# Kernel tuning notes

Hardware: AMD Instinct MI355X
Metric: run time of the kernel (lower is better)

## Reference

```python
import jax, jax.numpy as jnp
import numpy as np

B, T, D = 2, 2048, 1024
HV, HK = 16, 8
DK, DV = 64, 64
K_DIM = HK * DK          # 512
V_DIM = HV * DV          # 1024
CONV_DIM = 2 * K_DIM + V_DIM  # 2048
KS = 4                   # short-conv kernel size
EPS = 1e-6               # rms_norm_eps / l2norm eps


def setup_inputs() -> dict:
    key = jax.random.key(0)
    ks = jax.random.split(key, 9)
    g = lambda k, shape, sc: (jax.random.normal(k, shape, jnp.float32) * sc)
    return {
        "hidden_states": g(ks[0], (B, T, D), 1.0),
        "W_qkv": g(ks[1], (D, CONV_DIM), 0.02),
        "W_z": g(ks[2], (D, V_DIM), 0.02),
        "W_b": g(ks[3], (D, HV), 0.02),
        "W_a": g(ks[4], (D, HV), 0.02),
        "dt_bias": jnp.ones((HV,), jnp.float32),
        "A_log": jnp.log(jax.random.uniform(ks[5], (HV,), jnp.float32, 1e-3, 16.0)),
        "conv_w": g(ks[6], (CONV_DIM, KS), 0.2),
        "norm_w": jnp.ones((DV,), jnp.float32),
        "W_out": g(ks[7], (V_DIM, D), 0.02),
    }


def _causal_conv_silu(x, w):
    # depthwise causal conv1d over time, followed by SiLU (FLA ShortConvolution default)
    # x: [B,T,C], w: [C,KS]
    xp = jnp.pad(x, ((0, 0), (KS - 1, 0), (0, 0)))
    y = sum(xp[:, i:i + x.shape[1], :] * w[:, i] for i in range(KS))
    return jax.nn.silu(y)


def _l2norm(x):
    return x * jax.lax.rsqrt(jnp.sum(x * x, -1, keepdims=True) + EPS)


def _forward(hidden_states, W_qkv, W_z, W_b, W_a, dt_bias, A_log, conv_w, norm_w, W_out):
    b_, t_ = hidden_states.shape[:2]
    mixed_qkv = hidden_states @ W_qkv                       # [B,T,conv_dim]
    z = (hidden_states @ W_z).reshape(b_, t_, HV, DV)       # gate branch
    beta = jax.nn.sigmoid(hidden_states @ W_b)              # [B,T,HV]
    g = -jnp.exp(A_log) * jax.nn.softplus(hidden_states @ W_a + dt_bias)  # [B,T,HV]

    mixed_qkv = _causal_conv_silu(mixed_qkv, conv_w)
    q, k, v = jnp.split(mixed_qkv, [K_DIM, 2 * K_DIM], axis=-1)
    q = q.reshape(b_, t_, HK, DK)
    k = k.reshape(b_, t_, HK, DK)
    v = v.reshape(b_, t_, HV, DV)
    # GQA expansion of q/k to the value-head count
    rep = HV // HK
    q = jnp.repeat(q, rep, axis=2)
    k = jnp.repeat(k, rep, axis=2)
    # l2-norm on q/k in kernel; q additionally scaled by 1/sqrt(dk)
    q = _l2norm(q) * (DK ** -0.5)
    k = _l2norm(k)

    # gated delta-rule recurrence over time (state S: [B,HV,DK,DV])
    qT = q.transpose(1, 0, 2, 3)
    kT = k.transpose(1, 0, 2, 3)
    vT = v.transpose(1, 0, 2, 3)
    gT = g.transpose(1, 0, 2)
    bT = beta.transpose(1, 0, 2)

    def step(S, xs):
        q_t, k_t, v_t, g_t, b_t = xs
        S = S * jnp.exp(g_t)[..., None, None]
        kv = jnp.einsum('bhk,bhkv->bhv', k_t, S)
        S = S + jnp.einsum('bhk,bhv->bhkv', k_t, (v_t - kv) * b_t[..., None])
        o_t = jnp.einsum('bhk,bhkv->bhv', q_t, S)
        return S, o_t

    S0 = jnp.zeros((b_, HV, DK, DV), jnp.float32)
    _, oT = jax.lax.scan(step, S0, (qT, kT, vT, gT, bT))
    o = oT.transpose(1, 0, 2, 3)                            # [B,T,HV,DV]

    # gated RMSNorm: rmsnorm(o) * weight * silu(z)
    var = jnp.mean(o * o, axis=-1, keepdims=True)
    o = o * jax.lax.rsqrt(var + EPS) * norm_w * jax.nn.silu(z)

    return o.reshape(b_, t_, V_DIM) @ W_out


def reference(hidden_states, W_qkv, W_z, W_b, W_a, dt_bias, A_log, conv_w, norm_w, W_out):
    return _forward(hidden_states, W_qkv, W_z, W_b, W_a, dt_bias, A_log, conv_w, norm_w, W_out)
```

## Files before the change

kernel.cpp:

```cpp
#include <hip/hip_runtime.h>
#include <hip/hip_bf16.h>


typedef unsigned short u16;
typedef float f32x4 __attribute__((ext_vector_type(4)));
typedef short bf16x8 __attribute__((ext_vector_type(8)));
typedef u16 u16x4 __attribute__((ext_vector_type(4)));
typedef const __attribute__((address_space(1))) void* gptr_t;
typedef __attribute__((address_space(3))) void* lptr_t;

#define B_    2
#define T_    2048
#define HV_   16
#define HK_   8
#define NC_   32
#define BT_   4096
#define QKVZ_ 3072
#define NCOL_ 3200

__device__ __forceinline__ u16 f2bf(float f) {
  return __builtin_bit_cast(u16, __float2bfloat16(f));
}
__device__ __forceinline__ float bf2f(u16 u) {
  return __bfloat162float(__builtin_bit_cast(__hip_bfloat16, u));
}
__device__ __forceinline__ float sigm(float x) { return 1.f / (1.f + __expf(-x)); }

__global__ __launch_bounds__(256) void k_cast_hs(const float* __restrict__ in,
                                                 u16* __restrict__ out) {
  int i = (blockIdx.x * 256 + threadIdx.x) * 4;
  float4 v = *(const float4*)(in + i);
  u16x4 o; o.x = f2bf(v.x); o.y = f2bf(v.y); o.z = f2bf(v.z); o.w = f2bf(v.w);
  *(u16x4*)(out + i) = o;
}

__global__ __launch_bounds__(256) void k_tcast(const float* __restrict__ src,
                                               u16* __restrict__ dst, int R, int C) {
  __shared__ float tile[32][33];
  int c0 = blockIdx.x * 32, r0 = blockIdx.y * 32;
  int cx = threadIdx.x & 31, ry = threadIdx.x >> 5;
#pragma unroll
  for (int j = 0; j < 4; ++j)
    tile[ry * 4 + j][cx] = src[(long)(r0 + ry * 4 + j) * C + c0 + cx];
  __syncthreads();
#pragma unroll
  for (int j = 0; j < 4; ++j)
    dst[(long)(c0 + ry * 4 + j) * R + r0 + cx] = f2bf(tile[cx][ry * 4 + j]);
}

__global__ __launch_bounds__(256) void k_wcatT(const float* __restrict__ Wqkv,
                                               const float* __restrict__ Wz,
                                               const float* __restrict__ Wb,
                                               const float* __restrict__ Wa,
                                               u16* __restrict__ dst) {
  __shared__ float tile[32][33];
  int n0 = blockIdx.x * 32, k0 = blockIdx.y * 32;
  int cx = threadIdx.x & 31, ry = threadIdx.x >> 5;
#pragma unroll
  for (int j = 0; j < 4; ++j) {
    int kk = k0 + ry * 4 + j;
    int n = n0 + cx;
    float v;
    if (n < 2048)      v = Wqkv[(long)kk * 2048 + n];
    else if (n < 3072) v = Wz[(long)kk * 1024 + (n - 2048)];
    else if (n < 3088) v = Wb[kk * 16 + (n - 3072)];
    else if (n < 3104) v = Wa[kk * 16 + (n - 3088)];
    else               v = 0.f;
    tile[ry * 4 + j][cx] = v;
  }
  __syncthreads();
#pragma unroll
  for (int j = 0; j < 4; ++j)
    dst[(long)(n0 + ry * 4 + j) * 1024 + k0 + cx] = f2bf(tile[cx][ry * 4 + j]);
}

__global__ __launch_bounds__(256) void k_gemm(const u16* __restrict__ A,
                                              const u16* __restrict__ Bt,
                                              u16* __restrict__ C0,
                                              float* __restrict__ C1,
                                              int M, int N, int K, int mode) {
  __shared__ u16 As[128 * 64];
  __shared__ u16 Bs[128 * 64];
  int tid = threadIdx.x;
  int wid = tid >> 6, lane = tid & 63;
  int row0 = blockIdx.y * 128, col0 = blockIdx.x * 128;
  int wr = wid >> 1, wc = wid & 1;
  f32x4 acc[4][4];
#pragma unroll
  for (int m = 0; m < 4; ++m)
#pragma unroll
    for (int n = 0; n < 4; ++n) acc[m][n] = (f32x4){0.f, 0.f, 0.f, 0.f};

  int srow = lane >> 3;
  int skoff = (lane & 7) * 8;

  for (int k0 = 0; k0 < K; k0 += 64) {
#pragma unroll
    for (int it = 0; it < 4; ++it) {
      int seg = wid * 4 + it;
      int r = seg * 8 + srow;
      const u16* gA = A + (long)(row0 + r) * K + k0 + skoff;
      const u16* gB = Bt + (long)(col0 + r) * K + k0 + skoff;
      __builtin_amdgcn_global_load_lds((gptr_t)gA, (lptr_t)(As + seg * 512), 16, 0, 0);
      __builtin_amdgcn_global_load_lds((gptr_t)gB, (lptr_t)(Bs + seg * 512), 16, 0, 0);
    }
    asm volatile("s_waitcnt vmcnt(0)" ::: "memory");
    __syncthreads();
#pragma unroll
    for (int ks = 0; ks < 2; ++ks) {
      bf16x8 af[4], bfr[4];
      int kk = ks * 32 + (lane >> 4) * 8;
      int rA = wr * 64 + (lane & 15);
      int rB = wc * 64 + (lane & 15);
#pragma unroll
      for (int m = 0; m < 4; ++m) af[m] = *(const bf16x8*)(As + (rA + m * 16) * 64 + kk);
#pragma unroll
      for (int n = 0; n < 4; ++n) bfr[n] = *(const bf16x8*)(Bs + (rB + n * 16) * 64 + kk);
#pragma unroll
      for (int m = 0; m < 4; ++m)
#pragma unroll
        for (int n = 0; n < 4; ++n)
          acc[m][n] = __builtin_amdgcn_mfma_f32_16x16x32_bf16(af[m], bfr[n], acc[m][n], 0, 0, 0);
    }
    __syncthreads();
  }
#pragma unroll
  for (int m = 0; m < 4; ++m)
#pragma unroll
    for (int n = 0; n < 4; ++n)
#pragma unroll
      for (int r = 0; r < 4; ++r) {
        int row = row0 + wr * 64 + m * 16 + (lane >> 4) * 4 + r;
        int col = col0 + wc * 64 + n * 16 + (lane & 15);
        float v = acc[m][n][r];
        if (mode == 0) {
          if (col < QKVZ_) C0[(long)row * QKVZ_ + col] = f2bf(v);
          else             C1[(long)row * 128 + (col - QKVZ_)] = v;
        } else {
          C1[(long)row * N + col] = v;
        }
      }
}

__global__ __launch_bounds__(64) void k_conv(const u16* __restrict__ qkvz,
                                             const float* __restrict__ ba,
                                             const float* __restrict__ convw,
                                             const float* __restrict__ Alog,
                                             const float* __restrict__ dtb,
                                             u16* __restrict__ qn, u16* __restrict__ kn,
                                             u16* __restrict__ vb,
                                             float* __restrict__ beta, float* __restrict__ gb) {
  int bt = blockIdx.x;
  int t = bt & 2047;
  int l = threadIdx.x;
  long rb = (long)bt * QKVZ_;
#pragma unroll 1
  for (int j = 0; j < 32; ++j) {
    int c = j * 64 + l;
    float4 w = *(const float4*)(convw + c * 4);
    float a = 0.f;
#pragma unroll
    for (int d = 0; d < 4; ++d) {
      int tt = t - 3 + d;
      float x = (tt >= 0) ? bf2f(qkvz[rb + (long)(tt - t) * QKVZ_ + c]) : 0.f;
      a += x * ((const float*)&w)[d];
    }
    float y = a * sigm(a);
    if (j < 16) {
      float ss = y * y;
#pragma unroll
      for (int m = 1; m < 64; m <<= 1) ss += __shfl_xor(ss, m);
      float sc = rsqrtf(ss + 1e-6f);
      if (j < 8) qn[((long)bt * 8 + j) * 64 + l] = f2bf(y * sc * 0.125f);
      else       kn[((long)bt * 8 + (j - 8)) * 64 + l] = f2bf(y * sc);
    } else {
      vb[((long)bt * 16 + (j - 16)) * 64 + l] = f2bf(y);
    }
  }
  if (l < 16) {
    float xb = ba[(long)bt * 128 + l];
    beta[bt * 16 + l] = sigm(xb);
    float xa = ba[(long)bt * 128 + 16 + l] + dtb[l];
    float sp = (xa > 20.f) ? xa : log1pf(__expf(xa));
    gb[bt * 16 + l] = -__expf(Alog[l]) * sp;
  }
}

__global__ __launch_bounds__(256) void k_cpk2(const u16* __restrict__ qn,
                                              const u16* __restrict__ kn,
                                              const u16* __restrict__ vb,
                                              const float* __restrict__ beta,
                                              const float* __restrict__ gb,
                                              float* __restrict__ Gbuf,
                                              u16* __restrict__ TKTb,
                                              u16* __restrict__ WlTb, u16* __restrict__ MTb,
                                              u16* __restrict__ Pb, u16* __restrict__ Bb) {
  int c = blockIdx.x, hv = blockIdx.y, b = blockIdx.z;
  int hk = hv >> 1;
  int bh = b * HV_ + hv;
  int tid = threadIdx.x;
  int wv = tid >> 6, lane = tid & 63;
  int frow = lane & 15, fk = (lane >> 4) * 8;

  __shared__ __align__(16) char smem[78848];
  u16* Ks   = (u16*)smem;
  u16* Qs   = (u16*)(smem + 9216);
  u16* Ktt  = Qs;
  u16* As_  = (u16*)(smem + 18432);
  u16* RHSt = (u16*)(smem + 27648);
  u16* Xt   = (u16*)(smem + 46080);
  u16* T4   = (u16*)(smem + 64512);
  u16* Yl   = (u16*)(smem + 68608);
  __shared__ float Gl[64];
  __shared__ float Bl[64];

  long tbase = (long)b * T_ + c * 64;
  long tile = ((long)bh * NC_ + c) * 4096;

  if (tid < 64) {
    Gl[tid] = gb[(tbase + tid) * HV_ + hv];
    Bl[tid] = beta[(tbase + tid) * HV_ + hv];
  }
  if (tid == 0) {
    float s = 0.f;
    for (int i = 0; i < 64; ++i) { s += Gl[i]; Gl[i] = s; }
  }
  if (tid < 64) Gbuf[((long)bh * NC_ + c) * 64 + tid] = Gl[tid];
  for (int e = tid; e < 4608; e += 256) ((float*)Xt)[e] = 0.f;
  for (int e = tid; e < 2560; e += 256) ((float*)Yl)[e] = 0.f;
  for (int e = tid; e < 4096; e += 256) {
    int i = e >> 6, k = e & 63;
    Ks[i * 72 + k] = kn[(tbase + i) * 512 + hk * 64 + k];
    Qs[i * 72 + k] = qn[(tbase + i) * 512 + hk * 64 + k];
  }
  __syncthreads();

  {
    bf16x8 aKs[2];
#pragma unroll
    for (int ks = 0; ks < 2; ++ks)
      aKs[ks] = *(const bf16x8*)&Ks[(wv * 16 + frow) * 72 + ks * 32 + fk];
    f32x4 accM[4], accA[4];
#pragma unroll
    for (int nt = 0; nt < 4; ++nt) { accM[nt] = (f32x4){0,0,0,0}; accA[nt] = (f32x4){0,0,0,0}; }
#pragma unroll
    for (int ks = 0; ks < 2; ++ks) {
#pragma unroll
      for (int nt = 0; nt < 4; ++nt) {
        bf16x8 bq = *(const bf16x8*)&Qs[(nt * 16 + frow) * 72 + ks * 32 + fk];
        bf16x8 bk = *(const bf16x8*)&Ks[(nt * 16 + frow) * 72 + ks * 32 + fk];
        accM[nt] = __builtin_amdgcn_mfma_f32_16x16x32_bf16(aKs[ks], bq, accM[nt], 0, 0, 0);
        accA[nt] = __builtin_amdgcn_mfma_f32_16x16x32_bf16(aKs[ks], bk, accA[nt], 0, 0, 0);
      }
    }
#pragma unroll
    for (int nt = 0; nt < 4; ++nt) {
      int i = nt * 16 + frow;
#pragma unroll
      for (int r = 0; r < 4; ++r) {
        int s = wv * 16 + (lane >> 4) * 4 + r;
        float val = (s <= i) ? accM[nt][r] * __expf(Gl[i] - Gl[s]) : 0.f;
        MTb[tile + s * 64 + i] = f2bf(val);
      }
    }
#pragma unroll
    for (int nt = 0; nt < 4; ++nt) {
      int s = nt * 16 + frow;
#pragma unroll
      for (int r = 0; r < 4; ++r) {
        int i = wv * 16 + (lane >> 4) * 4 + r;
        float val = (s < i) ? Bl[i] * __expf(Gl[i] - Gl[s]) * accA[nt][r] : 0.f;
        As_[i * 72 + s] = f2bf(val);
      }
    }
  }

  for (int e = tid; e < 4096; e += 256) {
    int i = e >> 6, v = e & 63;
    RHSt[v * 72 + i] = f2bf(Bl[i] * bf2f(vb[(tbase + i) * 1024 + hv * 64 + v]));
  }
  for (int e = tid; e < 4096; e += 256) {
    int i = e >> 6, k = e & 63;
    RHSt[(64 + k) * 72 + i] = f2bf(Bl[i] * __expf(Gl[i]) * bf2f(Ks[i * 72 + k]));
  }
  __syncthreads();

  {
    if (lane < 16) {
      int cc = lane;
      float Tc[16];
#pragma unroll
      for (int j = 0; j < 16; ++j) Tc[j] = (j == cc) ? 1.f : 0.f;
#pragma unroll
      for (int s = 0; s < 15; ++s)
#pragma unroll
        for (int i = s + 1; i < 16; ++i) {
          float a = bf2f(As_[(wv * 16 + i) * 72 + wv * 16 + s]);
          Tc[i] -= a * Tc[s];
        }
#pragma unroll
      for (int i = 0; i < 16; ++i) T4[(wv * 16 + i) * 32 + cc] = f2bf(Tc[i]);
    } else if (lane < 32) {
      int c2 = lane - 16;
#pragma unroll
      for (int i = 0; i < 16; ++i) T4[(wv * 16 + i) * 32 + 16 + c2] = 0;
    }
  }
  __syncthreads();

#pragma unroll 1
  for (int bb = 0; bb < 4; ++bb) {
    f32x4 uacc[2];
    uacc[0] = (f32x4){0,0,0,0}; uacc[1] = (f32x4){0,0,0,0};
#pragma unroll
    for (int ks = 0; ks < 2; ++ks) {
      bf16x8 bfr = *(const bf16x8*)&As_[(bb * 16 + frow) * 72 + ks * 32 + fk];
#pragma unroll
      for (int mt = 0; mt < 2; ++mt) {
        bf16x8 aa = *(const bf16x8*)&Xt[((wv * 2 + mt) * 16 + frow) * 72 + ks * 32 + fk];
        uacc[mt] = __builtin_amdgcn_mfma_f32_16x16x32_bf16(aa, bfr, uacc[mt], 0, 0, 0);
      }
    }
#pragma unroll
    for (int mt = 0; mt < 2; ++mt)
#pragma unroll
      for (int r = 0; r < 4; ++r) {
        int vr = (wv * 2 + mt) * 16 + (lane >> 4) * 4 + r;
        float y = bf2f(RHSt[vr * 72 + bb * 16 + frow]) - uacc[mt][r];
        Yl[vr * 40 + frow] = f2bf(y);
      }
    __syncthreads();
    {
      bf16x8 tb = *(const bf16x8*)&T4[(bb * 16 + frow) * 32 + fk];
      f32x4 zacc[2];
      zacc[0] = (f32x4){0,0,0,0}; zacc[1] = (f32x4){0,0,0,0};
#pragma unroll
      for (int mt = 0; mt < 2; ++mt) {
        bf16x8 aa = *(const bf16x8*)&Yl[((wv * 2 + mt) * 16 + frow) * 40 + fk];
        zacc[mt] = __builtin_amdgcn_mfma_f32_16x16x32_bf16(aa, tb, zacc[mt], 0, 0, 0);
      }
#pragma unroll
      for (int mt = 0; mt < 2; ++mt)
#pragma unroll
        for (int r = 0; r < 4; ++r) {
          int vr = (wv * 2 + mt) * 16 + (lane >> 4) * 4 + r;
          Xt[vr * 72 + bb * 16 + frow] = f2bf(zacc[mt][r]);
        }
    }
    __syncthreads();
  }

  float gend = Gl[63];
  for (int e = tid; e < 4096; e += 256) {
    int i = e >> 6, r = e & 63;
    Ktt[r * 72 + i] = f2bf(__expf(gend - Gl[i]) * bf2f(Ks[i * 72 + r]));
  }
#pragma unroll
  for (int t8 = 0; t8 < 2; ++t8) {
    int seg = tid + t8 * 256;
    int row = seg >> 2, s4 = (seg & 3) * 16;
    bf16x8 x0 = *(const bf16x8*)&Xt[row * 72 + s4];
    bf16x8 x1 = *(const bf16x8*)&Xt[row * 72 + s4 + 8];
    u16* dst = (row < 64) ? (WlTb + tile + row * 64 + s4)
                          : (TKTb + tile + (long)(row - 64) * 64 + s4);
    *(bf16x8*)dst = x0;
    *(bf16x8*)(dst + 8) = x1;
  }
  __syncthreads();

  {
    f32x4 acc[4];
#pragma unroll
    for (int nt = 0; nt < 4; ++nt) acc[nt] = (f32x4){0,0,0,0};
#pragma unroll
    for (int ks = 0; ks < 2; ++ks) {
      bf16x8 aa = *(const bf16x8*)&Ktt[(wv * 16 + frow) * 72 + ks * 32 + fk];
#pragma unroll
      for (int nt = 0; nt < 4; ++nt) {
        bf16x8 bfr = *(const bf16x8*)&Xt[(nt * 16 + frow) * 72 + ks * 32 + fk];
        acc[nt] = __builtin_amdgcn_mfma_f32_16x16x32_bf16(aa, bfr, acc[nt], 0, 0, 0);
      }
    }
#pragma unroll
    for (int nt = 0; nt < 4; ++nt) {
      int v = nt * 16 + frow;
#pragma unroll
      for (int r = 0; r < 4; ++r) {
        int rr = wv * 16 + (lane >> 4) * 4 + r;
        Bb[tile + rr * 64 + v] = f2bf(acc[nt][r]);
      }
    }
  }
  {
    f32x4 acc[4];
#pragma unroll
    for (int nt = 0; nt < 4; ++nt) acc[nt] = (f32x4){0,0,0,0};
#pragma unroll
    for (int ks = 0; ks < 2; ++ks) {
      bf16x8 aa = *(const bf16x8*)&Xt[(64 + wv * 16 + frow) * 72 + ks * 32 + fk];
#pragma unroll
      for (int nt = 0; nt < 4; ++nt) {
        bf16x8 bfr = *(const bf16x8*)&Ktt[(nt * 16 + frow) * 72 + ks * 32 + fk];
        acc[nt] = __builtin_amdgcn_mfma_f32_16x16x32_bf16(aa, bfr, acc[nt], 0, 0, 0);
      }
    }
#pragma unroll
    for (int nt = 0; nt < 4; ++nt) {
      int rr = nt * 16 + frow;
#pragma unroll
      for (int r = 0; r < 4; ++r) {
        int k2 = wv * 16 + (lane >> 4) * 4 + r;
        Pb[tile + k2 * 64 + rr] = f2bf(acc[nt][r]);
      }
    }
  }
}

__global__ __launch_bounds__(256) void k_seq2(const u16* __restrict__ Pb,
                                              const u16* __restrict__ Bb,
                                              const float* __restrict__ Gbuf,
                                              u16* __restrict__ Stb) {
  int vblk = blockIdx.x, bh = blockIdx.y;
  int tid = threadIdx.x;
  __shared__ u16 Abf[2][4096];
  __shared__ u16 Bbf[2][512];
  __shared__ float S_lds[64][10];
  __shared__ float gam[NC_];
  int i_ = tid & 63, vg = tid >> 6;
  int wv = tid >> 6, ln = tid & 63;
  if (tid < NC_) gam[tid] = __expf(Gbuf[((long)bh * NC_ + tid) * 64 + 63]);
  for (int e = tid; e < 640; e += 256) ((float*)S_lds)[e] = 0.f;
  float a0 = 0.f, a1 = 0.f;
  {
    long tl = (long)bh * NC_ * 4096;
    const u16* gA = Pb + tl + wv * 512 + ln * 8;
    __builtin_amdgcn_global_load_lds((gptr_t)gA, (lptr_t)&Abf[0][wv * 512], 16, 0, 0);
    __builtin_amdgcn_global_load_lds((gptr_t)(gA + 2048), (lptr_t)&Abf[0][2048 + wv * 512], 16, 0, 0);
    int ii = tid >> 2, vp = tid & 3;
    const u16* gB = Bb + tl + ii * 64 + vblk * 8 + vp * 2;
    __builtin_amdgcn_global_load_lds((gptr_t)gB, (lptr_t)&Bbf[0][wv * 128], 4, 0, 0);
  }
  for (int c = 0; c < NC_; ++c) {
    int cur = c & 1;
    asm volatile("s_waitcnt vmcnt(0)" ::: "memory");
    __syncthreads();
    if (c + 1 < NC_) {
      long tl = ((long)bh * NC_ + c + 1) * 4096;
      const u16* gA = Pb + tl + wv * 512 + ln * 8;
      __builtin_amdgcn_global_load_lds((gptr_t)gA, (lptr_t)&Abf[cur ^ 1][wv * 512], 16, 0, 0);
      __builtin_amdgcn_global_load_lds((gptr_t)(gA + 2048), (lptr_t)&Abf[cur ^ 1][2048 + wv * 512], 16, 0, 0);
      int ii = tid >> 2, vp = tid & 3;
      const u16* gB = Bb + tl + ii * 64 + vblk * 8 + vp * 2;
      __builtin_amdgcn_global_load_lds((gptr_t)gB, (lptr_t)&Bbf[cur ^ 1][wv * 128], 4, 0, 0);
    }
    {
      long stile = ((long)bh * NC_ + c) * 4096;
      int v0 = vblk * 8 + vg * 2;
      Stb[stile + (long)v0 * 64 + i_] = f2bf(a0);
      Stb[stile + (long)(v0 + 1) * 64 + i_] = f2bf(a1);
    }
    float g = gam[c];
    float n0 = 0.f, n1 = 0.f;
#pragma unroll 8
    for (int k = 0; k < 64; ++k) {
      float p = bf2f(Abf[cur][k * 64 + i_]);
      float2 sv = *(const float2*)&S_lds[k][vg * 2];
      n0 += p * sv.x;
      n1 += p * sv.y;
    }
    float b0 = bf2f(Bbf[cur][i_ * 8 + vg * 2]);
    float b1 = bf2f(Bbf[cur][i_ * 8 + vg * 2 + 1]);
    a0 = g * a0 - n0 + b0;
    a1 = g * a1 - n1 + b1;
    __syncthreads();
    S_lds[i_][vg * 2] = a0;
    S_lds[i_][vg * 2 + 1] = a1;
  }
}

__global__ __launch_bounds__(256) void k_ok2(const u16* __restrict__ MTb,
                                             const u16* __restrict__ TKTb,
                                             const u16* __restrict__ WlTb,
                                             const u16* __restrict__ Stb,
                                             const u16* __restrict__ qn,
                                             const float* __restrict__ Gbuf,
                                             float* __restrict__ O) {
  int c = blockIdx.x, hv = blockIdx.y, b = blockIdx.z;
  int bh = b * HV_ + hv, hk = hv >> 1;
  int tid = threadIdx.x;
  __shared__ float TKt[64][68];
  __shared__ float Ss[64][68];
  __shared__ float Ws[64][68];
  __shared__ float Qt[64][68];
  __shared__ float Gl[64];
  long tile = ((long)bh * NC_ + c) * 4096;
  long tbase = (long)b * T_ + c * 64;
  if (tid < 64) Gl[tid] = Gbuf[((long)bh * NC_ + c) * 64 + tid];
  __syncthreads();
  for (int e = tid; e < 4096; e += 256)
    TKt[e >> 6][e & 63] = bf2f(TKTb[tile + e]);
  for (int e = tid; e < 4096; e += 256) {
    int i = e >> 6, k = e & 63;
    Qt[k][i] = __expf(Gl[i]) * bf2f(qn[(tbase + i) * 512 + hk * 64 + k]);
  }
  for (int e = tid; e < 4096; e += 256) {
    int v = e >> 6, x = e & 63;
    Ss[x][v] = bf2f(Stb[tile + e]);
    Ws[x][v] = bf2f(WlTb[tile + e]);
  }
  __syncthreads();
  int tx = tid & 15, ty = tid >> 4;
  int i0 = ty * 4, v0 = tx * 4;
  float w[4][4];
#pragma unroll
  for (int r = 0; r < 4; ++r) *(f32x4*)w[r] = *(const f32x4*)&Ws[i0 + r][v0];
  for (int k = 0; k < 64; ++k) {
    f32x4 tk = *(const f32x4*)&TKt[k][i0];
    f32x4 sv = *(const f32x4*)&Ss[k][v0];
#pragma unroll
    for (int r = 0; r < 4; ++r)
#pragma unroll
      for (int q = 0; q < 4; ++q) w[r][q] -= tk[r] * sv[q];
  }
  __syncthreads();
#pragma unroll
  for (int r = 0; r < 4; ++r) *(f32x4*)&Ws[i0 + r][v0] = *(const f32x4*)w[r];
  for (int e = tid; e < 4096; e += 256)
    TKt[e >> 6][e & 63] = bf2f(MTb[tile + e]);
  __syncthreads();
  float o[4][4] = {};
  for (int s = 0; s < 64; ++s) {
    f32x4 mv = *(const f32x4*)&TKt[s][i0];
    f32x4 wv = *(const f32x4*)&Ws[s][v0];
#pragma unroll
    for (int r = 0; r < 4; ++r)
#pragma unroll
      for (int q = 0; q < 4; ++q) o[r][q] += mv[r] * wv[q];
  }
  for (int k = 0; k < 64; ++k) {
    f32x4 qv = *(const f32x4*)&Qt[k][i0];
    f32x4 sv = *(const f32x4*)&Ss[k][v0];
#pragma unroll
    for (int r = 0; r < 4; ++r)
#pragma unroll
      for (int q = 0; q < 4; ++q) o[r][q] += qv[r] * sv[q];
  }
#pragma unroll
  for (int r = 0; r < 4; ++r) {
    float4 o4 = make_float4(o[r][0], o[r][1], o[r][2], o[r][3]);
    *(float4*)&O[((tbase + i0 + r) * HV_ + hv) * 64 + v0] = o4;
  }
}

__global__ __launch_bounds__(256) void k_rms(const float* __restrict__ O,
                                             const u16* __restrict__ qkvz,
                                             const float* __restrict__ normw,
                                             u16* __restrict__ on) {
  int bt = blockIdx.x;
  int tid = threadIdx.x;
  __shared__ float ps[256];
  __shared__ float rstd[16];
  float4 o4 = *(const float4*)&O[(long)bt * 1024 + tid * 4];
  ps[tid] = o4.x * o4.x + o4.y * o4.y + o4.z * o4.z + o4.w * o4.w;
  __syncthreads();
  if (tid < 16) {
    float s = 0.f;
#pragma unroll
    for (int u = 0; u < 16; ++u) s += ps[tid * 16 + u];
    rstd[tid] = rsqrtf(s * (1.f / 64.f) + 1e-6f);
  }
  __syncthreads();
  float rs = rstd[tid >> 4];
  u16x4 ov;
#pragma unroll
  for (int j = 0; j < 4; ++j) {
    int idx = tid * 4 + j;
    float z = bf2f(qkvz[(long)bt * QKVZ_ + 2048 + idx]);
    float val = ((const float*)&o4)[j] * rs * normw[idx & 63] * (z * sigm(z));
    ((u16*)&ov)[j] = f2bf(val);
  }
  *(u16x4*)(on + (long)bt * 1024 + tid * 4) = ov;
}

extern "C" void kernel_launch(void* const* d_in, const int* in_sizes, int n_in,
                              void* d_out, int out_size, void* d_ws, size_t ws_size,
                              hipStream_t stream) {
  const float* hs    = (const float*)d_in[0];
  const float* Wqkv  = (const float*)d_in[1];
  const float* Wz    = (const float*)d_in[2];
  const float* Wb    = (const float*)d_in[3];
  const float* Wa    = (const float*)d_in[4];
  const float* dtb   = (const float*)d_in[5];
  const float* Alog  = (const float*)d_in[6];
  const float* convw = (const float*)d_in[7];
  const float* normw = (const float*)d_in[8];
  const float* Wout  = (const float*)d_in[9];
  float* out = (float*)d_out;

  char* p = (char*)d_ws;
  auto take = [&](size_t bytes) {
    char* q = p;
    p += (bytes + 255) & ~(size_t)255;
    return (void*)q;
  };
  u16*   qkvz  = (u16*)take((size_t)BT_ * QKVZ_ * 2);
  float* ba    = (float*)take((size_t)BT_ * 128 * 4);
  u16*   hsb   = (u16*)take((size_t)BT_ * 1024 * 2);
  u16*   wcatT = (u16*)take((size_t)NCOL_ * 1024 * 2);
  u16*   woutT = (u16*)take((size_t)1024 * 1024 * 2);
  u16*   qn    = (u16*)take((size_t)BT_ * 512 * 2);
  u16*   kn    = (u16*)take((size_t)BT_ * 512 * 2);
  u16*   vbuf  = (u16*)take((size_t)BT_ * 1024 * 2);
  float* beta  = (float*)take((size_t)BT_ * 16 * 4);
  float* gbuf  = (float*)take((size_t)BT_ * 16 * 4);
  float* Gcum  = (float*)take((size_t)1024 * 64 * 4);
  u16*   TKTb  = (u16*)take((size_t)1024 * 4096 * 2);
  u16*   WlTb  = (u16*)take((size_t)1024 * 4096 * 2);
  u16*   MTb   = (u16*)take((size_t)1024 * 4096 * 2);
  u16*   Pb    = (u16*)take((size_t)1024 * 4096 * 2);
  u16*   Bb    = (u16*)take((size_t)1024 * 4096 * 2);
  u16*   Stb   = (u16*)take((size_t)1024 * 4096 * 2);
  float* Obuf  = (float*)take((size_t)BT_ * 1024 * 4);
  u16*   onb   = (u16*)take((size_t)BT_ * 1024 * 2);

  k_cast_hs<<<dim3(4096), dim3(256), 0, stream>>>(hs, hsb);
  k_wcatT<<<dim3(100, 32), dim3(256), 0, stream>>>(Wqkv, Wz, Wb, Wa, wcatT);
  k_tcast<<<dim3(32, 32), dim3(256), 0, stream>>>(Wout, woutT, 1024, 1024);
  k_gemm<<<dim3(25, 32), dim3(256), 0, stream>>>(hsb, wcatT, qkvz, ba, 4096, NCOL_, 1024, 0);
  k_conv<<<dim3(4096), dim3(64), 0, stream>>>(qkvz, ba, convw, Alog, dtb, qn, kn, vbuf, beta, gbuf);
  k_cpk2<<<dim3(32, 16, 2), dim3(256), 0, stream>>>(qn, kn, vbuf, beta, gbuf, Gcum, TKTb, WlTb, MTb, Pb, Bb);
  k_seq2<<<dim3(8, 32), dim3(256), 0, stream>>>(Pb, Bb, Gcum, Stb);
  k_ok2<<<dim3(32, 16, 2), dim3(256), 0, stream>>>(MTb, TKTb, WlTb, Stb, qn, Gcum, Obuf);
  k_rms<<<dim3(4096), dim3(256), 0, stream>>>(Obuf, qkvz, normw, onb);
  k_gemm<<<dim3(8, 32), dim3(256), 0, stream>>>(onb, woutT, (u16*)nullptr, out, 4096, 1024, 1024, 1);
}
```

Before: 363.0 us.

## Replace input projection GEMM with 256x256 pipelined LDS-DMA MFMA kernel

```diff
diff --git a/kernel.cpp b/kernel.cpp
--- a/kernel.cpp
+++ b/kernel.cpp
@@ -16,7 +16,7 @@
 #define NC_   32
 #define BT_   4096
 #define QKVZ_ 3072
-#define NCOL_ 3200
+#define NPAD_ 3328
 
 __device__ __forceinline__ u16 f2bf(float f) {
   return __builtin_bit_cast(u16, __float2bfloat16(f));
@@ -74,11 +74,118 @@
     dst[(long)(n0 + ry * 4 + j) * 1024 + k0 + cx] = f2bf(tile[cx][ry * 4 + j]);
 }
 
+__global__ __launch_bounds__(512, 1) void k_g1(const u16* __restrict__ A,
+                                               const u16* __restrict__ Bt,
+                                               u16* __restrict__ C0,
+                                               float* __restrict__ C1) {
+  extern __shared__ u16 smem[];
+  const int K = 1024;
+  int tid = threadIdx.x;
+  int wv = tid >> 6, lane = tid & 63;
+  int wm = wv >> 2, wn = wv & 3;
+  int frow = lane & 15, kq = lane >> 4;
+  long row0 = blockIdx.y * 256, col0 = blockIdx.x * 256;
+
+  f32x4 acc[8][4];
+#pragma unroll
+  for (int m = 0; m < 8; ++m)
+#pragma unroll
+    for (int n = 0; n < 4; ++n) acc[m][n] = (f32x4){0.f, 0.f, 0.f, 0.f};
+
+  auto stage = [&](int ts, int js) {
+    if (ts >= 16) return;
+    int op = js & 1, ks = js >> 1;
+    u16* base = smem + op * 32768 + (ts & 1) * 16384 + ks * 8192;
+    const u16* gsrc = op ? Bt : A;
+    long grow0 = op ? col0 : row0;
+#pragma unroll
+    for (int l = 0; l < 2; ++l) {
+      int c = wv * 128 + l * 64 + lane;
+      int cp = c ^ (((c >> 5) & 1) << 1);
+      int r = cp >> 2, kc = (cp & 3) * 8;
+      const u16* g = gsrc + (grow0 + r) * K + ts * 64 + ks * 32 + kc;
+      __builtin_amdgcn_global_load_lds((gptr_t)g, (lptr_t)(base + (wv * 128 + l * 64) * 8), 16, 0, 0);
+    }
+  };
+
+#define VM8 asm volatile("s_waitcnt vmcnt(8)" ::: "memory")
+#define VM4 asm volatile("s_waitcnt vmcnt(4)" ::: "memory")
+#define VM0 asm volatile("s_waitcnt vmcnt(0)" ::: "memory")
+#define VMN
+
+#define PHASE(T, KS, MH, STS, SJS, VMW)                                           \
+  {                                                                               \
+    bf16x8 af[4], bfr[4];                                                         \
+    const u16* Ab = smem + ((T) & 1) * 16384 + (KS) * 8192;                       \
+    const u16* Bb = smem + 32768 + ((T) & 1) * 16384 + (KS) * 8192;               \
+    _Pragma("unroll") for (int mt = 0; mt < 4; ++mt) {                            \
+      int R = wm * 128 + (MH) * 64 + mt * 16 + frow;                              \
+      int lin = R * 64 + kq * 16;                                                 \
+      af[mt] = *(const bf16x8*)((const char*)Ab + (lin ^ (((R >> 3) & 1) << 5))); \
+    }                                                                             \
+    _Pragma("unroll") for (int nt = 0; nt < 4; ++nt) {                            \
+      int R = wn * 64 + nt * 16 + frow;                                           \
+      int lin = R * 64 + kq * 16;                                                 \
+      bfr[nt] = *(const bf16x8*)((const char*)Bb + (lin ^ (((R >> 3) & 1) << 5)));\
+    }                                                                             \
+    stage(STS, SJS);                                                              \
+    VMW;                                                                          \
+    __syncthreads();                                                              \
+    __builtin_amdgcn_s_setprio(1);                                                \
+    _Pragma("unroll") for (int mt = 0; mt < 4; ++mt)                              \
+      _Pragma("unroll") for (int nt = 0; nt < 4; ++nt)                            \
+        acc[(MH) * 4 + mt][nt] = __builtin_amdgcn_mfma_f32_16x16x32_bf16(         \
+            af[mt], bfr[nt], acc[(MH) * 4 + mt][nt], 0, 0, 0);                    \
+    __builtin_amdgcn_s_setprio(0);                                                \
+    __syncthreads();                                                              \
+  }
+
+  stage(0, 0); stage(0, 1); stage(0, 2); stage(0, 3);
+  stage(1, 0); stage(1, 1);
+  VM8;
+  __syncthreads();
+
+#pragma unroll 1
+  for (int t = 0; t < 14; ++t) {
+    PHASE(t, 0, 0, t + 1, 2, VMN);
+    PHASE(t, 0, 1, t + 1, 3, VM8);
+    PHASE(t, 1, 0, t + 2, 0, VMN);
+    PHASE(t, 1, 1, t + 2, 1, VM8);
+  }
+  {
+    int t = 14;
+    PHASE(t, 0, 0, 15, 2, VMN);
+    PHASE(t, 0, 1, 15, 3, VM8);
+    PHASE(t, 1, 0, 16, 0, VMN);
+    PHASE(t, 1, 1, 16, 1, VM4);
+  }
+  {
+    int t = 15;
+    PHASE(t, 0, 0, 16, 2, VMN);
+    PHASE(t, 0, 1, 16, 3, VM0);
+    PHASE(t, 1, 0, 17, 0, VMN);
+    PHASE(t, 1, 1, 17, 1, VMN);
+  }
+#undef PHASE
+
+#pragma unroll
+  for (int m = 0; m < 8; ++m)
+#pragma unroll
+    for (int n = 0; n < 4; ++n)
+#pragma unroll
+      for (int r = 0; r < 4; ++r) {
+        long row = row0 + wm * 128 + m * 16 + kq * 4 + r;
+        long col = col0 + wn * 64 + n * 16 + frow;
+        float v = acc[m][n][r];
+        if (col < QKVZ_)      C0[row * QKVZ_ + col] = f2bf(v);
+        else if (col < 3200)  C1[row * 128 + (col - QKVZ_)] = v;
+      }
+}
+
 __global__ __launch_bounds__(256) void k_gemm(const u16* __restrict__ A,
                                               const u16* __restrict__ Bt,
-                                              u16* __restrict__ C0,
                                               float* __restrict__ C1,
-                                              int M, int N, int K, int mode) {
+                                              int M, int N, int K) {
   __shared__ u16 As[128 * 64];
   __shared__ u16 Bs[128 * 64];
   int tid = threadIdx.x;
@@ -132,13 +239,7 @@
       for (int r = 0; r < 4; ++r) {
         int row = row0 + wr * 64 + m * 16 + (lane >> 4) * 4 + r;
         int col = col0 + wc * 64 + n * 16 + (lane & 15);
-        float v = acc[m][n][r];
-        if (mode == 0) {
-          if (col < QKVZ_) C0[(long)row * QKVZ_ + col] = f2bf(v);
-          else             C1[(long)row * 128 + (col - QKVZ_)] = v;
-        } else {
-          C1[(long)row * N + col] = v;
-        }
+        C1[(long)row * N + col] = acc[m][n][r];
       }
 }
 
@@ -606,7 +707,7 @@
   u16*   qkvz  = (u16*)take((size_t)BT_ * QKVZ_ * 2);
   float* ba    = (float*)take((size_t)BT_ * 128 * 4);
   u16*   hsb   = (u16*)take((size_t)BT_ * 1024 * 2);
-  u16*   wcatT = (u16*)take((size_t)NCOL_ * 1024 * 2);
+  u16*   wcatT = (u16*)take((size_t)NPAD_ * 1024 * 2);
   u16*   woutT = (u16*)take((size_t)1024 * 1024 * 2);
   u16*   qn    = (u16*)take((size_t)BT_ * 512 * 2);
   u16*   kn    = (u16*)take((size_t)BT_ * 512 * 2);
@@ -624,13 +725,13 @@
   u16*   onb   = (u16*)take((size_t)BT_ * 1024 * 2);
 
   k_cast_hs<<<dim3(4096), dim3(256), 0, stream>>>(hs, hsb);
-  k_wcatT<<<dim3(100, 32), dim3(256), 0, stream>>>(Wqkv, Wz, Wb, Wa, wcatT);
+  k_wcatT<<<dim3(104, 32), dim3(256), 0, stream>>>(Wqkv, Wz, Wb, Wa, wcatT);
   k_tcast<<<dim3(32, 32), dim3(256), 0, stream>>>(Wout, woutT, 1024, 1024);
-  k_gemm<<<dim3(25, 32), dim3(256), 0, stream>>>(hsb, wcatT, qkvz, ba, 4096, NCOL_, 1024, 0);
+  k_g1<<<dim3(13, 16), dim3(512), 131072, stream>>>(hsb, wcatT, qkvz, ba);
   k_conv<<<dim3(4096), dim3(64), 0, stream>>>(qkvz, ba, convw, Alog, dtb, qn, kn, vbuf, beta, gbuf);
   k_cpk2<<<dim3(32, 16, 2), dim3(256), 0, stream>>>(qn, kn, vbuf, beta, gbuf, Gcum, TKTb, WlTb, MTb, Pb, Bb);
   k_seq2<<<dim3(8, 32), dim3(256), 0, stream>>>(Pb, Bb, Gcum, Stb);
   k_ok2<<<dim3(32, 16, 2), dim3(256), 0, stream>>>(MTb, TKTb, WlTb, Stb, qn, Gcum, Obuf);
   k_rms<<<dim3(4096), dim3(256), 0, stream>>>(Obuf, qkvz, normw, onb);
-  k_gemm<<<dim3(8, 32), dim3(256), 0, stream>>>(onb, woutT, (u16*)nullptr, out, 4096, 1024, 1024, 1);
-}
+  k_gemm<<<dim3(8, 32), dim3(256), 0, stream>>>(onb, woutT, out, 4096, 1024, 1024);
+}
```

Result: no change. 357.8 us (-1.4%).
